# Kernel optimization log

Measured on AMD Instinct MI355X. Metric: run time of the kernel, lower is better.

## Reference

```python
import jax, jax.numpy as jnp
import numpy as np

N, E, FX, H, B = 50000, 800000, 64, 64, 8
EPS = 1e-5


def _bn(h, gamma, beta):
    # BatchNorm1d in training mode: batch statistics, biased variance
    mu = h.mean(axis=0)
    var = ((h - mu) ** 2).mean(axis=0)
    return (h - mu) * jax.lax.rsqrt(var + EPS) * gamma + beta


def setup_inputs() -> dict:
    key = jax.random.key(0)
    ks = jax.random.split(key, 10)
    s = 0.05
    inp = {
        "x": jax.random.normal(ks[0], (N, FX), jnp.float32),
        "edge_index": jax.random.randint(ks[1], (2, E), 0, N),
        "edge_attr": jax.random.normal(ks[2], (E, H), jnp.float32),
        "u": jnp.zeros((1,), jnp.float32),
        "batch": jax.random.randint(ks[3], (E,), 0, B),
        # message_function params: Linear(FX+H->H), BN(H), Linear(H->H)
        "w1m": jax.random.normal(ks[4], (FX + H, H), jnp.float32) * s,
        "b1m": jnp.zeros((H,), jnp.float32),
        "gamma_m": jnp.ones((H,), jnp.float32),
        "beta_m": jnp.zeros((H,), jnp.float32),
        "w2m": jax.random.normal(ks[5], (H, H), jnp.float32) * s,
        "b2m": jnp.zeros((H,), jnp.float32),
        # node_mlp params: Linear(FX+H->H), BN(H), Linear(H->H)
        "w1n": jax.random.normal(ks[6], (FX + H, H), jnp.float32) * s,
        "b1n": jnp.zeros((H,), jnp.float32),
        "gamma_n": jnp.ones((H,), jnp.float32),
        "beta_n": jnp.zeros((H,), jnp.float32),
        "w2n": jax.random.normal(ks[7], (H, H), jnp.float32) * s,
        "b2n": jnp.zeros((H,), jnp.float32),
    }
    return inp


def reference(x, edge_index, edge_attr, u, batch,
              w1m, b1m, gamma_m, beta_m, w2m, b2m,
              w1n, b1n, gamma_n, beta_n, w2n, b2n):
    send_idx, rec_idx = edge_index[0], edge_index[1]
    n = x.shape[0]
    # gather sender node features, concat with edge features: [E, FX+H]
    m = jnp.concatenate([x[send_idx], edge_attr], axis=1)
    # message MLP: Linear -> BN -> ReLU -> Linear
    m = jax.nn.relu(_bn(m @ w1m + b1m, gamma_m, beta_m)) @ w2m + b2m
    # scatter_mean over receiving node index
    sums = jax.ops.segment_sum(m, rec_idx, num_segments=n)
    cnt = jax.ops.segment_sum(jnp.ones((m.shape[0],), m.dtype), rec_idx, num_segments=n)
    agg = sums / jnp.maximum(cnt, 1.0)[:, None]
    # node MLP on [x, aggregated messages]
    h = jnp.concatenate([x, agg], axis=1)
    return jax.nn.relu(_bn(h @ w1n + b1n, gamma_n, beta_n)) @ w2n + b2n
```

## Files before the change

### kernel.cpp

```cpp
#include <hip/hip_runtime.h>

typedef unsigned short bfu;
typedef unsigned int u32;
typedef __attribute__((ext_vector_type(8))) short bf16x8;
typedef __attribute__((ext_vector_type(4))) float f32x4;

#define N_NODES 50000
#define N_EDGES 800000
#define EPS_BN 1e-5f

__device__ __forceinline__ float bf2f(bfu u) { union { u32 i; float f; } v; v.i = ((u32)u) << 16; return v.f; }
__device__ __forceinline__ bfu f2bf(float f) {
    union { float f; u32 i; } v; v.f = f;
    u32 r = v.i + 0x7FFF + ((v.i >> 16) & 1);
    return (bfu)(r >> 16);
}
template<bool BF> __device__ __forceinline__ float ldf(const void* p, int i) {
    return BF ? bf2f(((const bfu*)p)[i]) : ((const float*)p)[i];
}

__global__ void k_detect(const void* gamma, int* flag) {
    if (blockIdx.x == 0 && threadIdx.x == 0)
        *flag = (((const bfu*)gamma)[0] != 0) ? 1 : 0;
}

__global__ void k_sent(u32* out, int n) {
    int i = blockIdx.x * blockDim.x + threadIdx.x;
    if (i < n) out[i] = 0x40E040E0u;
}

__global__ void k_zero(float* p, int n) {
    int i = blockIdx.x * blockDim.x + threadIdx.x;
    if (i < n) p[i] = 0.f;
}

__global__ void k_count(const int* __restrict__ rec, float* __restrict__ cnt, int n) {
    int i = blockIdx.x * blockDim.x + threadIdx.x;
    if (i < n) atomicAdd(&cnt[rec[i]], 1.0f);
}

template<bool BF>
__global__ void k_bnfin(const float* __restrict__ sum, const float* __restrict__ sq,
                        const void* __restrict__ gamma, const void* __restrict__ beta,
                        float* __restrict__ sc, float* __restrict__ sh, float count,
                        const int* __restrict__ flag) {
    if (*flag != (BF ? 1 : 0)) return;
    int c = threadIdx.x;
    float mu  = sum[c] / count;
    float var = sq[c] / count - mu * mu;
    float s = ldf<BF>(gamma, c) * rsqrtf(var + EPS_BN);
    sc[c] = s;
    sh[c] = ldf<BF>(beta, c) - mu * s;
}

__device__ __forceinline__ void split_arr(const float f[8], bf16x8& hi, bf16x8& lo) {
#pragma unroll
    for (int j = 0; j < 8; ++j) {
        bfu h = f2bf(f[j]);
        float r = f[j] - bf2f(h);
        hi[j] = (short)h;
        lo[j] = (short)f2bf(r);
    }
}
__device__ __forceinline__ void split8(const float* __restrict__ p, bf16x8& hi, bf16x8& lo) {
    float4 u = *(const float4*)p;
    float4 v = *(const float4*)(p + 4);
    float f[8] = {u.x, u.y, u.z, u.w, v.x, v.y, v.z, v.w};
    split_arr(f, hi, lo);
}

__device__ __forceinline__ void load_bfrags_f32(const float* __restrict__ wf, int l, int g,
                                                bf16x8 bhi[4][4], bf16x8 blo[4][4]) {
#pragma unroll
    for (int kt = 0; kt < 4; ++kt)
#pragma unroll
        for (int nt = 0; nt < 4; ++nt) {
            float f[8];
#pragma unroll
            for (int j = 0; j < 8; ++j)
                f[j] = wf[(kt * 32 + g * 8 + j) * 64 + nt * 16 + l];
            split_arr(f, bhi[kt][nt], blo[kt][nt]);
        }
}

__device__ __forceinline__ void edge_tile_f32s(const float* __restrict__ xf,
                                               const float* __restrict__ eaf,
                                               int e0, int my_snd, int l, int g,
                                               const bf16x8 bhi[4][4], const bf16x8 blo[4][4],
                                               f32x4 acc[4][4]) {
#pragma unroll
    for (int mt = 0; mt < 4; ++mt)
#pragma unroll
        for (int nt = 0; nt < 4; ++nt) acc[mt][nt] = (f32x4){0.f, 0.f, 0.f, 0.f};

#pragma unroll
    for (int kt = 0; kt < 4; ++kt) {
#pragma unroll
        for (int mt = 0; mt < 4; ++mt) {
            const int row = mt * 16 + l;
            const float* src;
            if (kt < 2) {
                const int snd = __shfl(my_snd, row);
                src = xf + (size_t)snd * 64 + kt * 32 + g * 8;
            } else {
                src = eaf + (size_t)(e0 + row) * 64 + (kt - 2) * 32 + g * 8;
            }
            bf16x8 ah, al;
            split8(src, ah, al);
#pragma unroll
            for (int nt = 0; nt < 4; ++nt) {
                acc[mt][nt] = __builtin_amdgcn_mfma_f32_16x16x32_bf16(ah, bhi[kt][nt], acc[mt][nt], 0, 0, 0);
                acc[mt][nt] = __builtin_amdgcn_mfma_f32_16x16x32_bf16(al, bhi[kt][nt], acc[mt][nt], 0, 0, 0);
                acc[mt][nt] = __builtin_amdgcn_mfma_f32_16x16x32_bf16(ah, blo[kt][nt], acc[mt][nt], 0, 0, 0);
            }
        }
    }
}

__global__ __launch_bounds__(256, 2) void k_stats_edge_f32s(
    const void* __restrict__ x, const int* __restrict__ send, const void* __restrict__ ea,
    const void* __restrict__ w1, const void* __restrict__ b1,
    float* __restrict__ colsum, float* __restrict__ colsq, const int* __restrict__ flag)
{
    if (*flag != 0) return;
    const int lane = threadIdx.x & 63;
    const int l = lane & 15, g = lane >> 4;
    const int wid = (blockIdx.x * blockDim.x + threadIdx.x) >> 6;
    const int nw  = (gridDim.x * blockDim.x) >> 6;
    const float* xf  = (const float*)x;
    const float* eaf = (const float*)ea;
    const float* b1f = (const float*)b1;

    bf16x8 bhi[4][4], blo[4][4];
    load_bfrags_f32((const float*)w1, l, g, bhi, blo);
    float bias[4];
#pragma unroll
    for (int nt = 0; nt < 4; ++nt) bias[nt] = b1f[nt * 16 + l];

    float sacc[4] = {0.f, 0.f, 0.f, 0.f}, qacc[4] = {0.f, 0.f, 0.f, 0.f};

    for (int t = wid; t < N_EDGES / 64; t += nw) {
        const int e0 = t * 64;
        const int my_snd = send[e0 + lane];
        f32x4 acc[4][4];
        edge_tile_f32s(xf, eaf, e0, my_snd, l, g, bhi, blo, acc);
#pragma unroll
        for (int nt = 0; nt < 4; ++nt) {
            float s = 0.f, q = 0.f;
#pragma unroll
            for (int mt = 0; mt < 4; ++mt)
#pragma unroll
                for (int r = 0; r < 4; ++r) {
                    float h = acc[mt][nt][r] + bias[nt];
                    s += h; q += h * h;
                }
            sacc[nt] += s; qacc[nt] += q;
        }
    }
#pragma unroll
    for (int nt = 0; nt < 4; ++nt) {
        float s = sacc[nt], q = qacc[nt];
        s += __shfl_xor(s, 16); s += __shfl_xor(s, 32);
        q += __shfl_xor(q, 16); q += __shfl_xor(q, 32);
        if (g == 0) {
            atomicAdd(&colsum[nt * 16 + l], s);
            atomicAdd(&colsq [nt * 16 + l], q);
        }
    }
}

__global__ __launch_bounds__(256, 2) void k_edge2_f32s(
    const void* __restrict__ x, const int* __restrict__ send, const int* __restrict__ rec,
    const void* __restrict__ ea, const void* __restrict__ w1, const void* __restrict__ b1,
    const float* __restrict__ sc, const float* __restrict__ sh,
    float* __restrict__ pagg, const int* __restrict__ flag)
{
    if (*flag != 0) return;
    const int lane = threadIdx.x & 63;
    const int l = lane & 15, g = lane >> 4;
    const int wid = (blockIdx.x * blockDim.x + threadIdx.x) >> 6;
    const int nw  = (gridDim.x * blockDim.x) >> 6;
    const float* xf  = (const float*)x;
    const float* eaf = (const float*)ea;
    const float* b1f = (const float*)b1;

    bf16x8 bhi[4][4], blo[4][4];
    load_bfrags_f32((const float*)w1, l, g, bhi, blo);
    float scl[4], shb[4];
#pragma unroll
    for (int nt = 0; nt < 4; ++nt) {
        const int c = nt * 16 + l;
        scl[nt] = sc[c];
        shb[nt] = b1f[c] * scl[nt] + sh[c];
    }

    for (int t = wid; t < N_EDGES / 64; t += nw) {
        const int e0 = t * 64;
        const int my_snd = send[e0 + lane];
        const int my_rv  = rec [e0 + lane];
        f32x4 acc[4][4];
        edge_tile_f32s(xf, eaf, e0, my_snd, l, g, bhi, blo, acc);
#pragma unroll
        for (int mt = 0; mt < 4; ++mt)
#pragma unroll
            for (int r = 0; r < 4; ++r) {
                const int m  = mt * 16 + g * 4 + r;
                const int rv = __shfl(my_rv, m);
                float* dst = pagg + (size_t)rv * 64 + l;
#pragma unroll
                for (int nt = 0; nt < 4; ++nt) {
                    float p = fmaxf(acc[mt][nt][r] * scl[nt] + shb[nt], 0.f);
                    atomicAdd(dst + nt * 16, p);
                }
            }
    }
}

__global__ __launch_bounds__(256, 2) void k_stats_node_f32s(
    const void* __restrict__ x, const float* __restrict__ agg,
    const void* __restrict__ w1, const void* __restrict__ b1,
    float* __restrict__ colsum, float* __restrict__ colsq, const int* __restrict__ flag)
{
    if (*flag != 0) return;
    const int lane = threadIdx.x & 63;
    const int l = lane & 15, g = lane >> 4;
    const int wid = (blockIdx.x * blockDim.x + threadIdx.x) >> 6;
    const int nw  = (gridDim.x * blockDim.x) >> 6;
    const float* xf  = (const float*)x;
    const float* b1f = (const float*)b1;

    bf16x8 bhi[4][4], blo[4][4];
    load_bfrags_f32((const float*)w1, l, g, bhi, blo);
    float bias[4];
#pragma unroll
    for (int nt = 0; nt < 4; ++nt) bias[nt] = b1f[nt * 16 + l];

    float sacc[4] = {0.f, 0.f, 0.f, 0.f}, qacc[4] = {0.f, 0.f, 0.f, 0.f};
    const int ntiles = (N_NODES + 63) / 64;

    for (int t = wid; t < ntiles; t += nw) {
        const int e0 = t * 64;
        f32x4 acc[4][4];
#pragma unroll
        for (int mt = 0; mt < 4; ++mt)
#pragma unroll
            for (int nt = 0; nt < 4; ++nt) acc[mt][nt] = (f32x4){0.f, 0.f, 0.f, 0.f};
#pragma unroll
        for (int kt = 0; kt < 4; ++kt) {
#pragma unroll
            for (int mt = 0; mt < 4; ++mt) {
                int v = e0 + mt * 16 + l;
                if (v >= N_NODES) v = N_NODES - 1;
                const float* src = (kt < 2)
                    ? xf  + (size_t)v * 64 + kt * 32 + g * 8
                    : agg + (size_t)v * 64 + (kt - 2) * 32 + g * 8;
                bf16x8 ah, al;
                split8(src, ah, al);
#pragma unroll
                for (int nt = 0; nt < 4; ++nt) {
                    acc[mt][nt] = __builtin_amdgcn_mfma_f32_16x16x32_bf16(ah, bhi[kt][nt], acc[mt][nt], 0, 0, 0);
                    acc[mt][nt] = __builtin_amdgcn_mfma_f32_16x16x32_bf16(al, bhi[kt][nt], acc[mt][nt], 0, 0, 0);
                    acc[mt][nt] = __builtin_amdgcn_mfma_f32_16x16x32_bf16(ah, blo[kt][nt], acc[mt][nt], 0, 0, 0);
                }
            }
        }
#pragma unroll
        for (int nt = 0; nt < 4; ++nt) {
            float s = 0.f, q = 0.f;
#pragma unroll
            for (int mt = 0; mt < 4; ++mt)
#pragma unroll
                for (int r = 0; r < 4; ++r) {
                    const int v = e0 + mt * 16 + g * 4 + r;
                    if (v < N_NODES) {
                        float h = acc[mt][nt][r] + bias[nt];
                        s += h; q += h * h;
                    }
                }
            sacc[nt] += s; qacc[nt] += q;
        }
    }
#pragma unroll
    for (int nt = 0; nt < 4; ++nt) {
        float s = sacc[nt], q = qacc[nt];
        s += __shfl_xor(s, 16); s += __shfl_xor(s, 32);
        q += __shfl_xor(q, 16); q += __shfl_xor(q, 32);
        if (g == 0) {
            atomicAdd(&colsum[nt * 16 + l], s);
            atomicAdd(&colsq [nt * 16 + l], q);
        }
    }
}

__device__ __forceinline__ void load_bfrags(const bfu* w1w, int l, int g, bf16x8 bfr[4][4]) {
#pragma unroll
    for (int kt = 0; kt < 4; ++kt)
#pragma unroll
        for (int nt = 0; nt < 4; ++nt) {
            bf16x8 v;
#pragma unroll
            for (int j = 0; j < 8; ++j)
                v[j] = (short)w1w[(kt * 32 + g * 8 + j) * 64 + nt * 16 + l];
            bfr[kt][nt] = v;
        }
}

__device__ __forceinline__ void edge_tile_mfma(const bfu* xw, const bfu* eaw,
                                               int e0, int my_snd, int l, int g,
                                               const bf16x8 bfr[4][4], f32x4 acc[4][4]) {
#pragma unroll
    for (int mt = 0; mt < 4; ++mt)
#pragma unroll
        for (int nt = 0; nt < 4; ++nt) acc[mt][nt] = (f32x4){0.f, 0.f, 0.f, 0.f};

#pragma unroll
    for (int kt = 0; kt < 4; ++kt) {
        bf16x8 afr[4];
#pragma unroll
        for (int mt = 0; mt < 4; ++mt) {
            const int row = mt * 16 + l;
            if (kt < 2) {
                const int snd = __shfl(my_snd, row);
                afr[mt] = *(const bf16x8*)(xw + (size_t)snd * 64 + kt * 32 + g * 8);
            } else {
                afr[mt] = *(const bf16x8*)(eaw + (size_t)(e0 + row) * 64 + (kt - 2) * 32 + g * 8);
            }
        }
#pragma unroll
        for (int mt = 0; mt < 4; ++mt)
#pragma unroll
            for (int nt = 0; nt < 4; ++nt)
                acc[mt][nt] = __builtin_amdgcn_mfma_f32_16x16x32_bf16(
                    afr[mt], bfr[kt][nt], acc[mt][nt], 0, 0, 0);
    }
}

__global__ __launch_bounds__(256) void k_stats_edge_mfma(
    const void* __restrict__ x, const int* __restrict__ send, const void* __restrict__ ea,
    const void* __restrict__ w1, const void* __restrict__ b1,
    float* __restrict__ colsum, float* __restrict__ colsq, const int* __restrict__ flag)
{
    if (*flag != 1) return;
    const int lane = threadIdx.x & 63;
    const int l = lane & 15, g = lane >> 4;
    const int wid = (blockIdx.x * blockDim.x + threadIdx.x) >> 6;
    const int nw  = (gridDim.x * blockDim.x) >> 6;
    const bfu* xw  = (const bfu*)x;
    const bfu* eaw = (const bfu*)ea;

    bf16x8 bfr[4][4];
    load_bfrags((const bfu*)w1, l, g, bfr);
    float bias[4];
#pragma unroll
    for (int nt = 0; nt < 4; ++nt) bias[nt] = bf2f(((const bfu*)b1)[nt * 16 + l]);

    float sacc[4] = {0.f, 0.f, 0.f, 0.f}, qacc[4] = {0.f, 0.f, 0.f, 0.f};

    for (int t = wid; t < N_EDGES / 64; t += nw) {
        const int e0 = t * 64;
        const int my_snd = send[e0 + lane];
        f32x4 acc[4][4];
        edge_tile_mfma(xw, eaw, e0, my_snd, l, g, bfr, acc);
#pragma unroll
        for (int nt = 0; nt < 4; ++nt) {
            float s = 0.f, q = 0.f;
#pragma unroll
            for (int mt = 0; mt < 4; ++mt)
#pragma unroll
                for (int r = 0; r < 4; ++r) {
                    float h = acc[mt][nt][r] + bias[nt];
                    s += h; q += h * h;
                }
            sacc[nt] += s; qacc[nt] += q;
        }
    }
#pragma unroll
    for (int nt = 0; nt < 4; ++nt) {
        float s = sacc[nt], q = qacc[nt];
        s += __shfl_xor(s, 16); s += __shfl_xor(s, 32);
        q += __shfl_xor(q, 16); q += __shfl_xor(q, 32);
        if (g == 0) {
            atomicAdd(&colsum[nt * 16 + l], s);
            atomicAdd(&colsq [nt * 16 + l], q);
        }
    }
}

__global__ __launch_bounds__(256) void k_edge2_mfma(
    const void* __restrict__ x, const int* __restrict__ send, const int* __restrict__ rec,
    const void* __restrict__ ea, const void* __restrict__ w1, const void* __restrict__ b1,
    const float* __restrict__ sc, const float* __restrict__ sh,
    float* __restrict__ pagg, const int* __restrict__ flag)
{
    if (*flag != 1) return;
    const int lane = threadIdx.x & 63;
    const int l = lane & 15, g = lane >> 4;
    const int wid = (blockIdx.x * blockDim.x + threadIdx.x) >> 6;
    const int nw  = (gridDim.x * blockDim.x) >> 6;
    const bfu* xw  = (const bfu*)x;
    const bfu* eaw = (const bfu*)ea;

    bf16x8 bfr[4][4];
    load_bfrags((const bfu*)w1, l, g, bfr);
    float scl[4], shb[4];
#pragma unroll
    for (int nt = 0; nt < 4; ++nt) {
        const int c = nt * 16 + l;
        const float bias = bf2f(((const bfu*)b1)[c]);
        scl[nt] = sc[c];
        shb[nt] = bias * scl[nt] + sh[c];
    }

    for (int t = wid; t < N_EDGES / 64; t += nw) {
        const int e0 = t * 64;
        const int my_snd = send[e0 + lane];
        const int my_rv  = rec [e0 + lane];
        f32x4 acc[4][4];
        edge_tile_mfma(xw, eaw, e0, my_snd, l, g, bfr, acc);
#pragma unroll
        for (int mt = 0; mt < 4; ++mt)
#pragma unroll
            for (int r = 0; r < 4; ++r) {
                const int m  = mt * 16 + g * 4 + r;
                const int rv = __shfl(my_rv, m);
                float* dst = pagg + (size_t)rv * 64 + l;
#pragma unroll
                for (int nt = 0; nt < 4; ++nt) {
                    float p = fmaxf(acc[mt][nt][r] * scl[nt] + shb[nt], 0.f);
                    atomicAdd(dst + nt * 16, p);
                }
            }
    }
}

template<bool BF>
__global__ __launch_bounds__(256) void k_agg(
    float* __restrict__ pagg, const float* __restrict__ cnt,
    const void* __restrict__ w2, const void* __restrict__ b2, const int* __restrict__ flag)
{
    if (*flag != (BF ? 1 : 0)) return;
    __shared__ float wlds[64 * 64];
    for (int i = threadIdx.x; i < 64 * 64; i += 256) wlds[i] = ldf<BF>(w2, i);
    __syncthreads();

    const int lane = threadIdx.x & 63;
    const int wid = (blockIdx.x * blockDim.x + threadIdx.x) >> 6;
    const int nw  = (gridDim.x * blockDim.x) >> 6;
    const float b = ldf<BF>(b2, lane);

    for (int v = wid; v < N_NODES; v += nw) {
        float acc = 0.f;
#pragma unroll 8
        for (int k = 0; k < 64; ++k) acc += pagg[v * 64 + k] * wlds[k * 64 + lane];
        const float c = cnt[v];
        pagg[v * 64 + lane] = (acc + c * b) / fmaxf(c, 1.0f);
    }
}

template<bool BF>
__global__ __launch_bounds__(256) void k_stats_node(
    const void* __restrict__ x, const float* __restrict__ agg,
    const void* __restrict__ w1, const void* __restrict__ b1,
    float* __restrict__ colsum, float* __restrict__ colsq, const int* __restrict__ flag)
{
    if (*flag != (BF ? 1 : 0)) return;
    __shared__ float wlds[128 * 64];
    for (int i = threadIdx.x; i < 128 * 64; i += 256) wlds[i] = ldf<BF>(w1, i);
    __syncthreads();

    const int lane = threadIdx.x & 63;
    const int wid = (blockIdx.x * blockDim.x + threadIdx.x) >> 6;
    const int nw  = (gridDim.x * blockDim.x) >> 6;
    const float bias = ldf<BF>(b1, lane);

    float sacc = 0.f, qacc = 0.f;
    for (int v = wid; v < N_NODES; v += nw) {
        float acc = bias;
#pragma unroll 8
        for (int k = 0; k < 64; ++k) acc += ldf<BF>(x, v * 64 + k) * wlds[k * 64 + lane];
#pragma unroll 8
        for (int k = 0; k < 64; ++k) acc += agg[v * 64 + k] * wlds[(64 + k) * 64 + lane];
        sacc += acc;
        qacc += acc * acc;
    }
    atomicAdd(&colsum[lane], sacc);
    atomicAdd(&colsq[lane], qacc);
}

template<bool BF>
__global__ __launch_bounds__(256) void k_out(
    const void* __restrict__ x, const float* __restrict__ agg,
    const void* __restrict__ w1, const void* __restrict__ b1,
    const void* __restrict__ w2, const void* __restrict__ b2,
    const float* __restrict__ sc, const float* __restrict__ sh,
    void* __restrict__ out, const int* __restrict__ flag)
{
    if (*flag != (BF ? 1 : 0)) return;
    __shared__ float w1lds[128 * 64];
    __shared__ float w2lds[64 * 64];
    for (int i = threadIdx.x; i < 128 * 64; i += 256) w1lds[i] = ldf<BF>(w1, i);
    for (int i = threadIdx.x; i < 64 * 64; i += 256)  w2lds[i] = ldf<BF>(w2, i);
    __syncthreads();

    const int lane = threadIdx.x & 63;
    const int wid = (blockIdx.x * blockDim.x + threadIdx.x) >> 6;
    const int nw  = (gridDim.x * blockDim.x) >> 6;
    const float bias = ldf<BF>(b1, lane);
    const float b2l  = ldf<BF>(b2, lane);
    const float scl = sc[lane], shl = sh[lane];

    for (int v = wid; v < N_NODES; v += nw) {
        float acc = bias;
#pragma unroll 8
        for (int k = 0; k < 64; ++k) acc += ldf<BF>(x, v * 64 + k) * w1lds[k * 64 + lane];
#pragma unroll 8
        for (int k = 0; k < 64; ++k) acc += agg[v * 64 + k] * w1lds[(64 + k) * 64 + lane];
        const float h = fmaxf(acc * scl + shl, 0.f);
        float res = b2l;
#pragma unroll 8
        for (int k = 0; k < 64; ++k) res += __shfl(h, k) * w2lds[k * 64 + lane];
        if (BF) ((bfu*)out)[v * 64 + lane] = f2bf(res);
        else    ((float*)out)[v * 64 + lane] = res;
    }
}

extern "C" __attribute__((visibility("default")))
void kernel_launch(void* const* d_in, const int* in_sizes, int n_in,
                   void* d_out, int out_size, void* d_ws, size_t ws_size,
                   hipStream_t stream)
{
    const void* x   = d_in[0];
    const int*  ei  = (const int*)d_in[1];
    const void* ea  = d_in[2];
    const void* w1m = d_in[5];
    const void* b1m = d_in[6];
    const void* gm  = d_in[7];
    const void* bm  = d_in[8];
    const void* w2m = d_in[9];
    const void* b2m = d_in[10];
    const void* w1n = d_in[11];
    const void* b1n = d_in[12];
    const void* gn  = d_in[13];
    const void* bn_ = d_in[14];
    const void* w2n = d_in[15];
    const void* b2n = d_in[16];

    char* ws = (char*)d_ws;
    float* pagg = (float*)(ws);
    float* cnt  = (float*)(ws + 12800000);
    float* st   = (float*)(ws + 13000000);
    int*   flag = (int*)(ws + 13002048);
    float* sum_m = st,       *sq_m = st + 64,  *sum_n = st + 128, *sq_n = st + 192;
    float* sc_m  = st + 256, *sh_m = st + 320, *sc_n  = st + 384, *sh_n = st + 448;

    const int* send = ei;
    const int* rec  = ei + N_EDGES;

    k_detect<<<1, 64, 0, stream>>>(gm, flag);
    const int nsent = out_size / 2;
    k_sent<<<(nsent + 255) / 256, 256, 0, stream>>>((u32*)d_out, nsent);
    const int zn = 3200000 + 50000 + 512;
    k_zero<<<(zn + 255) / 256, 256, 0, stream>>>(pagg, zn);
    k_count<<<(N_EDGES + 255) / 256, 256, 0, stream>>>(rec, cnt, N_EDGES);

    k_stats_edge_mfma<<<512, 256, 0, stream>>>(x, send, ea, w1m, b1m, sum_m, sq_m, flag);
    k_stats_edge_f32s<<<512, 256, 0, stream>>>(x, send, ea, w1m, b1m, sum_m, sq_m, flag);
    k_bnfin<true ><<<1, 64, 0, stream>>>(sum_m, sq_m, gm, bm, sc_m, sh_m, (float)N_EDGES, flag);
    k_bnfin<false><<<1, 64, 0, stream>>>(sum_m, sq_m, gm, bm, sc_m, sh_m, (float)N_EDGES, flag);
    k_edge2_mfma<<<512, 256, 0, stream>>>(x, send, rec, ea, w1m, b1m, sc_m, sh_m, pagg, flag);
    k_edge2_f32s<<<512, 256, 0, stream>>>(x, send, rec, ea, w1m, b1m, sc_m, sh_m, pagg, flag);
    k_agg<true ><<<256, 256, 0, stream>>>(pagg, cnt, w2m, b2m, flag);
    k_agg<false><<<256, 256, 0, stream>>>(pagg, cnt, w2m, b2m, flag);
    k_stats_node<true ><<<256, 256, 0, stream>>>(x, pagg, w1n, b1n, sum_n, sq_n, flag);
    k_stats_node_f32s<<<196, 256, 0, stream>>>(x, pagg, w1n, b1n, sum_n, sq_n, flag);
    k_bnfin<true ><<<1, 64, 0, stream>>>(sum_n, sq_n, gn, bn_, sc_n, sh_n, (float)N_NODES, flag);
    k_bnfin<false><<<1, 64, 0, stream>>>(sum_n, sq_n, gn, bn_, sc_n, sh_n, (float)N_NODES, flag);
    k_out<true ><<<256, 256, 0, stream>>>(x, pagg, w1n, b1n, w2n, b2n, sc_n, sh_n, d_out, flag);
    k_out<false><<<256, 256, 0, stream>>>(x, pagg, w1n, b1n, w2n, b2n, sc_n, sh_n, d_out, flag);
}
```

Before: 934.6 us.

## Move fp32 aggregation and node-output paths to split-bf16 MFMA, cache node hidden

The fp32 aggregation step (mean plus second message linear) gets a new kernel that uses split-bf16 MFMA instead of the generic templated path. The node stage now writes the pre-BN hidden activations into the output buffer, so the final kernel only applies BN, ReLU and the second linear from LDS weights rather than recomputing the first GEMM. The bf16 hi split becomes a cheap truncation instead of round-to-nearest, and the fp32 edge kernels are launched with more blocks. These changes trade extra global traffic for the hidden buffer and a slightly different hi/lo split for less recomputation and more parallelism.

Result: faster. 847.9 us (-9.3%).

```diff
diff --git a/kernel.cpp b/kernel.cpp
--- a/kernel.cpp
+++ b/kernel.cpp
@@ -56,9 +56,10 @@
 __device__ __forceinline__ void split_arr(const float f[8], bf16x8& hi, bf16x8& lo) {
 #pragma unroll
     for (int j = 0; j < 8; ++j) {
-        bfu h = f2bf(f[j]);
-        float r = f[j] - bf2f(h);
-        hi[j] = (short)h;
+        union { float f; u32 i; } v; v.f = f[j];
+        hi[j] = (short)(v.i >> 16);
+        union { u32 i; float f; } hf; hf.i = v.i & 0xFFFF0000u;
+        float r = f[j] - hf.f;
         lo[j] = (short)f2bf(r);
     }
 }
@@ -73,6 +74,19 @@
                                                 bf16x8 bhi[4][4], bf16x8 blo[4][4]) {
 #pragma unroll
     for (int kt = 0; kt < 4; ++kt)
+#pragma unroll
+        for (int nt = 0; nt < 4; ++nt) {
+            float f[8];
+#pragma unroll
+            for (int j = 0; j < 8; ++j)
+                f[j] = wf[(kt * 32 + g * 8 + j) * 64 + nt * 16 + l];
+            split_arr(f, bhi[kt][nt], blo[kt][nt]);
+        }
+}
+__device__ __forceinline__ void load_bfrags2_f32(const float* __restrict__ wf, int l, int g,
+                                                 bf16x8 bhi[2][4], bf16x8 blo[2][4]) {
+#pragma unroll
+    for (int kt = 0; kt < 2; ++kt)
 #pragma unroll
         for (int nt = 0; nt < 4; ++nt) {
             float f[8];
@@ -216,9 +230,67 @@
     }
 }
 
-__global__ __launch_bounds__(256, 2) void k_stats_node_f32s(
+__global__ __launch_bounds__(256, 2) void k_agg_f32s(
+    float* __restrict__ pagg, const float* __restrict__ cnt,
+    const void* __restrict__ w2, const void* __restrict__ b2, const int* __restrict__ flag)
+{
+    if (*flag != 0) return;
+    const int lane = threadIdx.x & 63;
+    const int l = lane & 15, g = lane >> 4;
+    const int wid = (blockIdx.x * blockDim.x + threadIdx.x) >> 6;
+    const int nw  = (gridDim.x * blockDim.x) >> 6;
+    const float* b2f = (const float*)b2;
+
+    bf16x8 bhi[2][4], blo[2][4];
+    load_bfrags2_f32((const float*)w2, l, g, bhi, blo);
+    float b2l[4];
+#pragma unroll
+    for (int nt = 0; nt < 4; ++nt) b2l[nt] = b2f[nt * 16 + l];
+
+    const int ntiles = (N_NODES + 63) / 64;
+    for (int t = wid; t < ntiles; t += nw) {
+        const int v0 = t * 64;
+        f32x4 acc[4][4];
+#pragma unroll
+        for (int mt = 0; mt < 4; ++mt)
+#pragma unroll
+            for (int nt = 0; nt < 4; ++nt) acc[mt][nt] = (f32x4){0.f, 0.f, 0.f, 0.f};
+#pragma unroll
+        for (int kt = 0; kt < 2; ++kt) {
+#pragma unroll
+            for (int mt = 0; mt < 4; ++mt) {
+                int v = v0 + mt * 16 + l;
+                if (v >= N_NODES) v = N_NODES - 1;
+                bf16x8 ah, al;
+                split8(pagg + (size_t)v * 64 + kt * 32 + g * 8, ah, al);
+#pragma unroll
+                for (int nt = 0; nt < 4; ++nt) {
+                    acc[mt][nt] = __builtin_amdgcn_mfma_f32_16x16x32_bf16(ah, bhi[kt][nt], acc[mt][nt], 0, 0, 0);
+                    acc[mt][nt] = __builtin_amdgcn_mfma_f32_16x16x32_bf16(al, bhi[kt][nt], acc[mt][nt], 0, 0, 0);
+                    acc[mt][nt] = __builtin_amdgcn_mfma_f32_16x16x32_bf16(ah, blo[kt][nt], acc[mt][nt], 0, 0, 0);
+                }
+            }
+        }
+#pragma unroll
+        for (int mt = 0; mt < 4; ++mt)
+#pragma unroll
+            for (int r = 0; r < 4; ++r) {
+                const int v = v0 + mt * 16 + g * 4 + r;
+                if (v < N_NODES) {
+                    const float c = cnt[v];
+                    const float inv = 1.0f / fmaxf(c, 1.0f);
+#pragma unroll
+                    for (int nt = 0; nt < 4; ++nt)
+                        pagg[(size_t)v * 64 + nt * 16 + l] = (acc[mt][nt][r] + c * b2l[nt]) * inv;
+                }
+            }
+    }
+}
+
+__global__ __launch_bounds__(256, 2) void k_h_node_f32s(
     const void* __restrict__ x, const float* __restrict__ agg,
     const void* __restrict__ w1, const void* __restrict__ b1,
+    float* __restrict__ hbuf,
     float* __restrict__ colsum, float* __restrict__ colsq, const int* __restrict__ flag)
 {
     if (*flag != 0) return;
@@ -239,7 +311,7 @@
     const int ntiles = (N_NODES + 63) / 64;
 
     for (int t = wid; t < ntiles; t += nw) {
-        const int e0 = t * 64;
+        const int v0 = t * 64;
         f32x4 acc[4][4];
 #pragma unroll
         for (int mt = 0; mt < 4; ++mt)
@@ -249,7 +321,7 @@
         for (int kt = 0; kt < 4; ++kt) {
 #pragma unroll
             for (int mt = 0; mt < 4; ++mt) {
-                int v = e0 + mt * 16 + l;
+                int v = v0 + mt * 16 + l;
                 if (v >= N_NODES) v = N_NODES - 1;
                 const float* src = (kt < 2)
                     ? xf  + (size_t)v * 64 + kt * 32 + g * 8
@@ -271,10 +343,11 @@
             for (int mt = 0; mt < 4; ++mt)
 #pragma unroll
                 for (int r = 0; r < 4; ++r) {
-                    const int v = e0 + mt * 16 + g * 4 + r;
+                    const int v = v0 + mt * 16 + g * 4 + r;
                     if (v < N_NODES) {
                         float h = acc[mt][nt][r] + bias[nt];
                         s += h; q += h * h;
+                        hbuf[(size_t)v * 64 + nt * 16 + l] = h;
                     }
                 }
             sacc[nt] += s; qacc[nt] += q;
@@ -289,6 +362,32 @@
             atomicAdd(&colsum[nt * 16 + l], s);
             atomicAdd(&colsq [nt * 16 + l], q);
         }
+    }
+}
+
+__global__ __launch_bounds__(256) void k_out2_f32(
+    const void* __restrict__ w2, const void* __restrict__ b2,
+    const float* __restrict__ sc, const float* __restrict__ sh,
+    float* __restrict__ out, const int* __restrict__ flag)
+{
+    if (*flag != 0) return;
+    __shared__ float wlds[64 * 64];
+    for (int i = threadIdx.x; i < 64 * 64; i += 256) wlds[i] = ((const float*)w2)[i];
+    __syncthreads();
+
+    const int lane = threadIdx.x & 63;
+    const int wid = (blockIdx.x * blockDim.x + threadIdx.x) >> 6;
+    const int nw  = (gridDim.x * blockDim.x) >> 6;
+    const float scl = sc[lane], shl = sh[lane];
+    const float b2l = ((const float*)b2)[lane];
+
+    for (int v = wid; v < N_NODES; v += nw) {
+        const float h1 = out[(size_t)v * 64 + lane];
+        const float h  = fmaxf(h1 * scl + shl, 0.f);
+        float res = b2l;
+#pragma unroll
+        for (int k = 0; k < 64; ++k) res += __shfl(h, k) * wlds[k * 64 + lane];
+        out[(size_t)v * 64 + lane] = res;
     }
 }
 
@@ -564,17 +663,17 @@
     k_count<<<(N_EDGES + 255) / 256, 256, 0, stream>>>(rec, cnt, N_EDGES);
 
     k_stats_edge_mfma<<<512, 256, 0, stream>>>(x, send, ea, w1m, b1m, sum_m, sq_m, flag);
-    k_stats_edge_f32s<<<512, 256, 0, stream>>>(x, send, ea, w1m, b1m, sum_m, sq_m, flag);
+    k_stats_edge_f32s<<<1563, 256, 0, stream>>>(x, send, ea, w1m, b1m, sum_m, sq_m, flag);
     k_bnfin<true ><<<1, 64, 0, stream>>>(sum_m, sq_m, gm, bm, sc_m, sh_m, (float)N_EDGES, flag);
     k_bnfin<false><<<1, 64, 0, stream>>>(sum_m, sq_m, gm, bm, sc_m, sh_m, (float)N_EDGES, flag);
     k_edge2_mfma<<<512, 256, 0, stream>>>(x, send, rec, ea, w1m, b1m, sc_m, sh_m, pagg, flag);
-    k_edge2_f32s<<<512, 256, 0, stream>>>(x, send, rec, ea, w1m, b1m, sc_m, sh_m, pagg, flag);
+    k_edge2_f32s<<<1563, 256, 0, stream>>>(x, send, rec, ea, w1m, b1m, sc_m, sh_m, pagg, flag);
     k_agg<true ><<<256, 256, 0, stream>>>(pagg, cnt, w2m, b2m, flag);
-    k_agg<false><<<256, 256, 0, stream>>>(pagg, cnt, w2m, b2m, flag);
+    k_agg_f32s<<<196, 256, 0, stream>>>(pagg, cnt, w2m, b2m, flag);
     k_stats_node<true ><<<256, 256, 0, stream>>>(x, pagg, w1n, b1n, sum_n, sq_n, flag);
-    k_stats_node_f32s<<<196, 256, 0, stream>>>(x, pagg, w1n, b1n, sum_n, sq_n, flag);
+    k_h_node_f32s<<<196, 256, 0, stream>>>(x, pagg, w1n, b1n, (float*)d_out, sum_n, sq_n, flag);
     k_bnfin<true ><<<1, 64, 0, stream>>>(sum_n, sq_n, gn, bn_, sc_n, sh_n, (float)N_NODES, flag);
     k_bnfin<false><<<1, 64, 0, stream>>>(sum_n, sq_n, gn, bn_, sc_n, sh_n, (float)N_NODES, flag);
     k_out<true ><<<256, 256, 0, stream>>>(x, pagg, w1n, b1n, w2n, b2n, sc_n, sh_n, d_out, flag);
-    k_out<false><<<256, 256, 0, stream>>>(x, pagg, w1n, b1n, w2n, b2n, sc_n, sh_n, d_out, flag);
-}
+    k_out2_f32<<<256, 256, 0, stream>>>(w2n, b2n, sc_n, sh_n, (float*)d_out, flag);
+}
```
